# Kernel tuning notes

Measured on AMD Instinct MI355X. Metric: run time of the kernel, lower is better.

Reference implementation:

```python
import jax, jax.numpy as jnp
import numpy as np

N = 50000        # nodes
E = 1_600_000    # edges (avg degree 32)
IN_DIM = 128
NUM_CONFS = 16
CONF_EMB = 4
HIDDEN = 64
OUT = 32


def setup_inputs() -> dict:
    key = jax.random.key(0)
    ks = jax.random.split(key, 8)
    x = jax.random.normal(ks[0], (N, IN_DIM), jnp.float32)
    conf_ids = jax.random.randint(ks[1], (N,), 0, NUM_CONFS)
    edge_index = jax.random.randint(ks[2], (2, E), 0, N)
    edge_weight = jax.random.uniform(ks[3], (E,), jnp.float32)
    # learned params
    conf_table = jax.random.normal(ks[4], (NUM_CONFS, CONF_EMB), jnp.float32) * 0.1
    W1 = jax.random.normal(ks[5], (IN_DIM + CONF_EMB, HIDDEN), jnp.float32) / np.sqrt(IN_DIM + CONF_EMB)
    b1 = jnp.zeros((HIDDEN,), jnp.float32)
    W2 = jax.random.normal(ks[6], (HIDDEN, OUT), jnp.float32) / np.sqrt(HIDDEN)
    b2 = jnp.zeros((OUT,), jnp.float32)
    return dict(x=x, conf_ids=conf_ids, edge_index=edge_index, edge_weight=edge_weight,
                conf_table=conf_table, W1=W1, b1=b1, W2=W2, b2=b2)


def _gcn_conv(h, W, b, row, col, w, n):
    """PyG GCNConv: symmetric norm with self-loops (loops already appended to row/col/w)."""
    deg = jax.ops.segment_sum(w, col, num_segments=n)              # weighted in-degree [N]
    dinv = jnp.where(deg > 0, jax.lax.rsqrt(deg), 0.0)             # D^{-1/2}
    norm = dinv[row] * w * dinv[col]                               # per-edge coefficient [E+N]
    hW = h @ W                                                     # [N, out]
    out = jax.ops.segment_sum(hW[row] * norm[:, None], col, num_segments=n)
    return out + b


def reference(x, conf_ids, edge_index, edge_weight, conf_table, W1, b1, W2, b2):
    row, col = edge_index[0], edge_index[1]
    # add self-loops once (same math for both conv layers)
    loop = jnp.arange(N)
    row = jnp.concatenate([row, loop])
    col = jnp.concatenate([col, loop])
    w = jnp.concatenate([edge_weight, jnp.ones((N,), edge_weight.dtype)])

    h = jnp.concatenate([x, conf_table[conf_ids]], axis=-1)        # [N, in+conf_emb]
    h = jax.nn.relu(_gcn_conv(h, W1, b1, row, col, w, N))
    return _gcn_conv(h, W2, b2, row, col, w, N)
```

## Files before the change

### kernel.cpp

```cpp
#include <hip/hip_runtime.h>
#include <hip/hip_fp16.h>

#define WSCALE   65535.0f
#define BKT_SHIFT 8
#define BKT_SIZE  256
#define SEGCAP    10240
#define EPB       4096
#define EPT       16
#define NT        64

__global__ void k_binA(const int* __restrict__ row, const int* __restrict__ col,
                       const float* __restrict__ w, int* __restrict__ cursor,
                       uint2* __restrict__ seg, int e) {
    __shared__ int hist[256];
    __shared__ int base[256];
    __shared__ int rank[256];
    int t = threadIdx.x;
    hist[t] = 0; rank[t] = 0;
    __syncthreads();
    int b0 = blockIdx.x * EPB;
    unsigned pay[EPT]; unsigned cc[EPT];
#pragma unroll
    for (int k = 0; k < EPT; ++k) {
        int i = b0 + k * 256 + t;
        if (i < e) {
            unsigned r  = (unsigned)row[i];
            unsigned c  = (unsigned)col[i];
            unsigned wq = __float2uint_rn(w[i] * WSCALE);
            pay[k] = r | (wq << 16);
            cc[k] = c;
            atomicAdd(&hist[c >> BKT_SHIFT], 1);
        } else cc[k] = 0xFFFFFFFFu;
    }
    __syncthreads();
    if (hist[t] > 0) base[t] = atomicAdd(&cursor[t], hist[t]);
    __syncthreads();
#pragma unroll
    for (int k = 0; k < EPT; ++k) {
        if (cc[k] != 0xFFFFFFFFu) {
            int b = cc[k] >> BKT_SHIFT;
            int pos = base[b] + atomicAdd(&rank[b], 1);
            if (pos < SEGCAP)
                seg[(size_t)b * SEGCAP + pos] = make_uint2(pay[k], cc[k] & (BKT_SIZE - 1));
        }
    }
}

__global__ void k_binB(const int* __restrict__ cursor, const uint2* __restrict__ seg,
                       unsigned* __restrict__ csr, int* __restrict__ begs,
                       int* __restrict__ cnts, float* __restrict__ dinv, int n) {
    __shared__ int hist[BKT_SIZE];
    __shared__ unsigned wsum[BKT_SIZE];
    __shared__ int begL[BKT_SIZE];
    __shared__ int rank[BKT_SIZE];
    __shared__ unsigned pay[SEGCAP];
    int b = blockIdx.x;
    int t = threadIdx.x;
    int nodes = min(BKT_SIZE, n - b * BKT_SIZE);
    int count = min(cursor[b], SEGCAP);
    hist[t] = 0; wsum[t] = 0; rank[t] = 0;
    __syncthreads();
    const uint2* sp = seg + (size_t)b * SEGCAP;
    for (int i = t; i < count; i += 256) {
        uint2 r = sp[i];
        atomicAdd(&hist[r.y], 1);
        atomicAdd(&wsum[r.y], r.x >> 16);
    }
    __syncthreads();
    int v = hist[t];
    begL[t] = v;
    __syncthreads();
    for (int off = 1; off < 256; off <<= 1) {
        int tv = 0;
        if (t >= off) tv = begL[t - off];
        __syncthreads();
        begL[t] += tv;
        __syncthreads();
    }
    int beg_excl = begL[t] - v;
    __syncthreads();
    begL[t] = beg_excl;
    __syncthreads();
    if (t < nodes) {
        int node = b * BKT_SIZE + t;
        begs[node] = b * SEGCAP + beg_excl;
        cnts[node] = v;
        dinv[node] = rsqrtf(1.0f + (float)wsum[t] * (1.0f / WSCALE));
    }
    for (int i = t; i < count; i += 256) {
        uint2 r = sp[i];
        int pos = begL[r.y] + atomicAdd(&rank[r.y], 1);
        pay[pos] = r.x;
    }
    __syncthreads();
    unsigned* cp = csr + (size_t)b * SEGCAP;
    for (int i = t; i < count; i += 256) cp[i] = pay[i];
}

__global__ void k_hw1(const float* __restrict__ x, const int* __restrict__ conf_ids,
                      const float* __restrict__ conf_table, const float* __restrict__ W1,
                      const float* __restrict__ dinv, __half* __restrict__ hW1s, int n) {
    __shared__ float xs[NT][128];
    __shared__ float cemb[NT][4];
    int t = threadIdx.x;
    int base = blockIdx.x * NT;
    for (int q = t; q < NT * 32; q += 256) {
        int node = base + (q >> 5);
        int k4 = (q & 31) * 4;
        float4 v = make_float4(0.f, 0.f, 0.f, 0.f);
        if (node < n) v = *(const float4*)(x + (size_t)node * 128 + k4);
        *(float4*)&xs[q >> 5][k4] = v;
    }
    if (t < NT) {
        int node = base + t;
        int cid = (node < n) ? conf_ids[node] : 0;
        float4 ce = *(const float4*)(conf_table + cid * 4);
        if (node >= n) ce = make_float4(0.f, 0.f, 0.f, 0.f);
        *(float4*)&cemb[t][0] = ce;
    }
    __syncthreads();
    int w = t >> 6, f = t & 63;
    int nb = w * 16;
    float acc[16];
#pragma unroll
    for (int m = 0; m < 16; ++m) acc[m] = 0.f;
    for (int kq = 0; kq < 32; ++kq) {
        int k = kq * 4;
        float w1a = W1[(k + 0) * 64 + f];
        float w1b = W1[(k + 1) * 64 + f];
        float w1c = W1[(k + 2) * 64 + f];
        float w1d = W1[(k + 3) * 64 + f];
#pragma unroll
        for (int m = 0; m < 16; ++m) {
            float4 xv = *(const float4*)&xs[nb + m][k];
            acc[m] += xv.x * w1a + xv.y * w1b + xv.z * w1c + xv.w * w1d;
        }
    }
    float wca = W1[128 * 64 + f], wcb = W1[129 * 64 + f];
    float wcc = W1[130 * 64 + f], wcd = W1[131 * 64 + f];
#pragma unroll
    for (int m = 0; m < 16; ++m) {
        float4 ce = *(const float4*)&cemb[nb + m][0];
        acc[m] += ce.x * wca + ce.y * wcb + ce.z * wcc + ce.w * wcd;
    }
#pragma unroll
    for (int m = 0; m < 16; ++m) {
        int node = base + nb + m;
        if (node < n) hW1s[(size_t)node * 64 + f] = __float2half_rn(acc[m] * dinv[node]);
    }
}

__global__ void k_agg1(const __half* __restrict__ hW1s, const int* __restrict__ begs,
                       const int* __restrict__ cnts, const unsigned* __restrict__ csr,
                       const float* __restrict__ dinv, const float* __restrict__ b1,
                       const float* __restrict__ W2, __half* __restrict__ hW2s, int n) {
    __shared__ float h1s[8][64];
    int t = threadIdx.x;
    int q  = t >> 5;
    int hl = t & 31;
    int nid = blockIdx.x * 8 + q;
    const half2* __restrict__ hrow = (const half2*)hW1s;
    float a0 = 0.f, a1 = 0.f, dn = 0.f;
    float2 sf = make_float2(0.f, 0.f);
    int c = 0;
    const unsigned* sp = csr;
    if (nid < n) {
        dn = dinv[nid];
        c = cnts[nid];
        sp = csr + begs[nid];
        sf = __half22float2(hrow[(size_t)nid * 32 + hl]);
    }
    int cmax = max(c, __shfl_xor(c, 32));
    int j = 0;
    for (; j + 4 <= cmax; j += 4) {
        unsigned s0 = sp[j], s1 = sp[j + 1], s2 = sp[j + 2], s3 = sp[j + 3];
        float w0 = (j + 0 < c) ? (float)(s0 >> 16) : 0.f;
        float w1 = (j + 1 < c) ? (float)(s1 >> 16) : 0.f;
        float w2 = (j + 2 < c) ? (float)(s2 >> 16) : 0.f;
        float w3 = (j + 3 < c) ? (float)(s3 >> 16) : 0.f;
        float2 v0 = __half22float2(hrow[(size_t)(s0 & 0xffffu) * 32 + hl]);
        float2 v1 = __half22float2(hrow[(size_t)(s1 & 0xffffu) * 32 + hl]);
        float2 v2 = __half22float2(hrow[(size_t)(s2 & 0xffffu) * 32 + hl]);
        float2 v3 = __half22float2(hrow[(size_t)(s3 & 0xffffu) * 32 + hl]);
        a0 += v0.x * w0 + v1.x * w1 + v2.x * w2 + v3.x * w3;
        a1 += v0.y * w0 + v1.y * w1 + v2.y * w2 + v3.y * w3;
    }
    for (; j < cmax; ++j) {
        unsigned s = sp[j];
        float ww = (j < c) ? (float)(s >> 16) : 0.f;
        float2 v = __half22float2(hrow[(size_t)(s & 0xffffu) * 32 + hl]);
        a0 += v.x * ww;
        a1 += v.y * ww;
    }
    float2 bb = *(const float2*)(b1 + 2 * hl);
    float h0 = fmaxf((sf.x + a0 * (1.0f / WSCALE)) * dn + bb.x, 0.0f);
    float h1v = fmaxf((sf.y + a1 * (1.0f / WSCALE)) * dn + bb.y, 0.0f);
    if (nid >= n) { h0 = 0.f; h1v = 0.f; }
    *(float2*)&h1s[q][2 * hl] = make_float2(h0, h1v);
    __syncthreads();
    float s = 0.f;
#pragma unroll
    for (int k = 0; k < 64; k += 4) {
        float4 hv = *(const float4*)&h1s[q][k];
        s += hv.x * W2[(k + 0) * 32 + hl];
        s += hv.y * W2[(k + 1) * 32 + hl];
        s += hv.z * W2[(k + 2) * 32 + hl];
        s += hv.w * W2[(k + 3) * 32 + hl];
    }
    if (nid < n) hW2s[(size_t)nid * 32 + hl] = __float2half_rn(s * dn);
}

__global__ void k_agg2(const __half* __restrict__ hW2s, const int* __restrict__ begs,
                       const int* __restrict__ cnts, const unsigned* __restrict__ csr,
                       const float* __restrict__ dinv, const float* __restrict__ b2,
                       float* __restrict__ out, int n) {
    int t = threadIdx.x;
    int g  = t >> 4;
    int hl = t & 15;
    int nid = blockIdx.x * 16 + g;
    const half2* __restrict__ hrow = (const half2*)hW2s;
    float a0 = 0.f, a1 = 0.f, dn = 0.f;
    float2 sf = make_float2(0.f, 0.f);
    int c = 0;
    const unsigned* sp = csr;
    if (nid < n) {
        dn = dinv[nid];
        c = cnts[nid];
        sp = csr + begs[nid];
        sf = __half22float2(hrow[(size_t)nid * 16 + hl]);
    }
    int cmax = max(c, __shfl_xor(c, 16));
    cmax = max(cmax, __shfl_xor(cmax, 32));
    int j = 0;
    for (; j + 4 <= cmax; j += 4) {
        unsigned s0 = sp[j], s1 = sp[j + 1], s2 = sp[j + 2], s3 = sp[j + 3];
        float w0 = (j + 0 < c) ? (float)(s0 >> 16) : 0.f;
        float w1 = (j + 1 < c) ? (float)(s1 >> 16) : 0.f;
        float w2 = (j + 2 < c) ? (float)(s2 >> 16) : 0.f;
        float w3 = (j + 3 < c) ? (float)(s3 >> 16) : 0.f;
        float2 v0 = __half22float2(hrow[(size_t)(s0 & 0xffffu) * 16 + hl]);
        float2 v1 = __half22float2(hrow[(size_t)(s1 & 0xffffu) * 16 + hl]);
        float2 v2 = __half22float2(hrow[(size_t)(s2 & 0xffffu) * 16 + hl]);
        float2 v3 = __half22float2(hrow[(size_t)(s3 & 0xffffu) * 16 + hl]);
        a0 += v0.x * w0 + v1.x * w1 + v2.x * w2 + v3.x * w3;
        a1 += v0.y * w0 + v1.y * w1 + v2.y * w2 + v3.y * w3;
    }
    for (; j < cmax; ++j) {
        unsigned s = sp[j];
        float ww = (j < c) ? (float)(s >> 16) : 0.f;
        float2 v = __half22float2(hrow[(size_t)(s & 0xffffu) * 16 + hl]);
        a0 += v.x * ww;
        a1 += v.y * ww;
    }
    if (nid < n) {
        float2 bb = *(const float2*)(b2 + 2 * hl);
        float o0 = (sf.x + a0 * (1.0f / WSCALE)) * dn + bb.x;
        float o1 = (sf.y + a1 * (1.0f / WSCALE)) * dn + bb.y;
        *(float2*)&out[(size_t)nid * 32 + 2 * hl] = make_float2(o0, o1);
    }
}

extern "C" void kernel_launch(void* const* d_in, const int* in_sizes, int n_in,
                              void* d_out, int out_size, void* d_ws, size_t ws_size,
                              hipStream_t stream) {
    const float* x          = (const float*)d_in[0];
    const int*   conf_ids   = (const int*)  d_in[1];
    const int*   eidx       = (const int*)  d_in[2];
    const float* ew         = (const float*)d_in[3];
    const float* conf_table = (const float*)d_in[4];
    const float* W1         = (const float*)d_in[5];
    const float* b1         = (const float*)d_in[6];
    const float* W2         = (const float*)d_in[7];
    const float* b2         = (const float*)d_in[8];
    float* out = (float*)d_out;

    const int n = in_sizes[1];
    const int e = in_sizes[3];
    const int* row = eidx;
    const int* col = eidx + e;
    const int nbkt = (n + BKT_SIZE - 1) / BKT_SIZE;

    char* ws = (char*)d_ws;
    size_t off = 0;
    auto alloc = [&](size_t bytes) -> char* {
        char* p = ws + off;
        off = (off + bytes + 255) & ~(size_t)255;
        return p;
    };
    int*      cursor = (int*)     alloc(256 * 4);
    uint2*    seg    = (uint2*)   alloc((size_t)nbkt * SEGCAP * 8);
    unsigned* csr    = (unsigned*)alloc((size_t)nbkt * SEGCAP * 4);
    int*      begs   = (int*)     alloc((size_t)n * 4);
    int*      cnts   = (int*)     alloc((size_t)n * 4);
    float*    dinv   = (float*)   alloc((size_t)n * 4);
    __half*   hW2s   = (__half*)  alloc((size_t)n * 32 * 2);
    __half*   hW1s   = (__half*)seg;

    const int B = 256;
    int ga  = (e + EPB - 1) / EPB;
    int gt  = (n + NT - 1) / NT;
    int g8  = (n + 7) / 8;
    int g16 = (n + 15) / 16;

    hipMemsetAsync(cursor, 0, 256 * 4, stream);
    k_binA<<<ga,   B, 0, stream>>>(row, col, ew, cursor, seg, e);
    k_binB<<<nbkt, B, 0, stream>>>(cursor, seg, csr, begs, cnts, dinv, n);
    k_hw1 <<<gt,   B, 0, stream>>>(x, conf_ids, conf_table, W1, dinv, hW1s, n);
    k_agg1<<<g8,   B, 0, stream>>>(hW1s, begs, cnts, csr, dinv, b1, W2, hW2s, n);
    k_agg2<<<g16,  B, 0, stream>>>(hW2s, begs, cnts, csr, dinv, b2, out, n);
}
```

Baseline: 145.1 us.

## Pad CSR rows to multiples of 8 and aggregate with fp16 weights and packed FMA

Edge weights are now stored as fp16 bits instead of 16-bit fixed point, so the gather loops can do half2 FMAs without an int-to-float conversion. Each node's CSR row is zero-padded to a multiple of 8 entries, which allows 16-byte uint4 loads of the edge list with one-block prefetch and removes per-edge bounds masks and the cross-lane max of counts. The costs are less accumulation precision from fp16 partial sums over 8 edges, extra padded CSR storage and writes, and possible over-reads past the segment end during prefetch.

Result: faster. 135.7 us (-6.5%).

```diff
diff --git a/kernel.cpp b/kernel.cpp
--- a/kernel.cpp
+++ b/kernel.cpp
@@ -1,7 +1,6 @@
 #include <hip/hip_runtime.h>
 #include <hip/hip_fp16.h>
 
-#define WSCALE   65535.0f
 #define BKT_SHIFT 8
 #define BKT_SIZE  256
 #define SEGCAP    10240
@@ -26,7 +25,7 @@
         if (i < e) {
             unsigned r  = (unsigned)row[i];
             unsigned c  = (unsigned)col[i];
-            unsigned wq = __float2uint_rn(w[i] * WSCALE);
+            unsigned wq = (unsigned)__half_as_ushort(__float2half_rn(w[i]));
             pay[k] = r | (wq << 16);
             cc[k] = c;
             atomicAdd(&hist[c >> BKT_SHIFT], 1);
@@ -50,7 +49,7 @@
                        unsigned* __restrict__ csr, int* __restrict__ begs,
                        int* __restrict__ cnts, float* __restrict__ dinv, int n) {
     __shared__ int hist[BKT_SIZE];
-    __shared__ unsigned wsum[BKT_SIZE];
+    __shared__ float wsumf[BKT_SIZE];
     __shared__ int begL[BKT_SIZE];
     __shared__ int rank[BKT_SIZE];
     __shared__ unsigned pay[SEGCAP];
@@ -58,43 +57,46 @@
     int t = threadIdx.x;
     int nodes = min(BKT_SIZE, n - b * BKT_SIZE);
     int count = min(cursor[b], SEGCAP);
-    hist[t] = 0; wsum[t] = 0; rank[t] = 0;
+    hist[t] = 0; wsumf[t] = 0.f; rank[t] = 0;
     __syncthreads();
     const uint2* sp = seg + (size_t)b * SEGCAP;
     for (int i = t; i < count; i += 256) {
         uint2 r = sp[i];
         atomicAdd(&hist[r.y], 1);
-        atomicAdd(&wsum[r.y], r.x >> 16);
+        atomicAdd(&wsumf[r.y], __half2float(__ushort_as_half((unsigned short)(r.x >> 16))));
     }
     __syncthreads();
     int v = hist[t];
-    begL[t] = v;
+    int vpad = (v + 7) & ~7;
+    begL[t] = vpad;
     __syncthreads();
     for (int off = 1; off < 256; off <<= 1) {
-        int tv = 0;
-        if (t >= off) tv = begL[t - off];
+        int tv = (t >= off) ? begL[t - off] : 0;
         __syncthreads();
         begL[t] += tv;
         __syncthreads();
     }
-    int beg_excl = begL[t] - v;
+    int beg_excl = begL[t] - vpad;
+    int ptot = min(begL[255], SEGCAP);
     __syncthreads();
     begL[t] = beg_excl;
     __syncthreads();
     if (t < nodes) {
         int node = b * BKT_SIZE + t;
         begs[node] = b * SEGCAP + beg_excl;
-        cnts[node] = v;
-        dinv[node] = rsqrtf(1.0f + (float)wsum[t] * (1.0f / WSCALE));
-    }
+        cnts[node] = vpad;
+        dinv[node] = rsqrtf(1.0f + wsumf[t]);
+    }
+    for (int i = t; i < ptot; i += 256) pay[i] = 0u;
+    __syncthreads();
     for (int i = t; i < count; i += 256) {
         uint2 r = sp[i];
         int pos = begL[r.y] + atomicAdd(&rank[r.y], 1);
-        pay[pos] = r.x;
+        if (pos < SEGCAP) pay[pos] = r.x;
     }
     __syncthreads();
     unsigned* cp = csr + (size_t)b * SEGCAP;
-    for (int i = t; i < count; i += 256) cp[i] = pay[i];
+    for (int i = t; i < ptot; i += 256) cp[i] = pay[i];
 }
 
 __global__ void k_hw1(const float* __restrict__ x, const int* __restrict__ conf_ids,
@@ -160,7 +162,7 @@
     int hl = t & 31;
     int nid = blockIdx.x * 8 + q;
     const half2* __restrict__ hrow = (const half2*)hW1s;
-    float a0 = 0.f, a1 = 0.f, dn = 0.f;
+    float dn = 0.f;
     float2 sf = make_float2(0.f, 0.f);
     int c = 0;
     const unsigned* sp = csr;
@@ -170,31 +172,29 @@
         sp = csr + begs[nid];
         sf = __half22float2(hrow[(size_t)nid * 32 + hl]);
     }
-    int cmax = max(c, __shfl_xor(c, 32));
-    int j = 0;
-    for (; j + 4 <= cmax; j += 4) {
-        unsigned s0 = sp[j], s1 = sp[j + 1], s2 = sp[j + 2], s3 = sp[j + 3];
-        float w0 = (j + 0 < c) ? (float)(s0 >> 16) : 0.f;
-        float w1 = (j + 1 < c) ? (float)(s1 >> 16) : 0.f;
-        float w2 = (j + 2 < c) ? (float)(s2 >> 16) : 0.f;
-        float w3 = (j + 3 < c) ? (float)(s3 >> 16) : 0.f;
-        float2 v0 = __half22float2(hrow[(size_t)(s0 & 0xffffu) * 32 + hl]);
-        float2 v1 = __half22float2(hrow[(size_t)(s1 & 0xffffu) * 32 + hl]);
-        float2 v2 = __half22float2(hrow[(size_t)(s2 & 0xffffu) * 32 + hl]);
-        float2 v3 = __half22float2(hrow[(size_t)(s3 & 0xffffu) * 32 + hl]);
-        a0 += v0.x * w0 + v1.x * w1 + v2.x * w2 + v3.x * w3;
-        a1 += v0.y * w0 + v1.y * w1 + v2.y * w2 + v3.y * w3;
-    }
-    for (; j < cmax; ++j) {
-        unsigned s = sp[j];
-        float ww = (j < c) ? (float)(s >> 16) : 0.f;
-        float2 v = __half22float2(hrow[(size_t)(s & 0xffffu) * 32 + hl]);
-        a0 += v.x * ww;
-        a1 += v.y * ww;
+    float a0 = 0.f, a1 = 0.f;
+    const half2 hz = __float2half2_rn(0.f);
+    uint4 sa = *(const uint4*)(sp);
+    uint4 sb = *(const uint4*)(sp + 4);
+    for (int j = 0; j < c; j += 8) {
+        uint4 na = *(const uint4*)(sp + j + 8);
+        uint4 nb = *(const uint4*)(sp + j + 12);
+        half2 acc0 = hz, acc1 = hz;
+#define STEP1(s, A) { half2 vv = hrow[(size_t)((s) & 0xffffu) * 32 + hl]; \
+                      half2 ww = __half2half2(__ushort_as_half((unsigned short)((s) >> 16))); \
+                      A = __hfma2(vv, ww, A); }
+        STEP1(sa.x, acc0) STEP1(sa.y, acc1) STEP1(sa.z, acc0) STEP1(sa.w, acc1)
+        STEP1(sb.x, acc0) STEP1(sb.y, acc1) STEP1(sb.z, acc0) STEP1(sb.w, acc1)
+#undef STEP1
+        float2 f0 = __half22float2(acc0);
+        float2 f1 = __half22float2(acc1);
+        a0 += f0.x + f1.x;
+        a1 += f0.y + f1.y;
+        sa = na; sb = nb;
     }
     float2 bb = *(const float2*)(b1 + 2 * hl);
-    float h0 = fmaxf((sf.x + a0 * (1.0f / WSCALE)) * dn + bb.x, 0.0f);
-    float h1v = fmaxf((sf.y + a1 * (1.0f / WSCALE)) * dn + bb.y, 0.0f);
+    float h0  = fmaxf((sf.x + a0) * dn + bb.x, 0.0f);
+    float h1v = fmaxf((sf.y + a1) * dn + bb.y, 0.0f);
     if (nid >= n) { h0 = 0.f; h1v = 0.f; }
     *(float2*)&h1s[q][2 * hl] = make_float2(h0, h1v);
     __syncthreads();
@@ -219,7 +219,7 @@
     int hl = t & 15;
     int nid = blockIdx.x * 16 + g;
     const half2* __restrict__ hrow = (const half2*)hW2s;
-    float a0 = 0.f, a1 = 0.f, dn = 0.f;
+    float dn = 0.f;
     float2 sf = make_float2(0.f, 0.f);
     int c = 0;
     const unsigned* sp = csr;
@@ -229,33 +229,30 @@
         sp = csr + begs[nid];
         sf = __half22float2(hrow[(size_t)nid * 16 + hl]);
     }
-    int cmax = max(c, __shfl_xor(c, 16));
-    cmax = max(cmax, __shfl_xor(cmax, 32));
-    int j = 0;
-    for (; j + 4 <= cmax; j += 4) {
-        unsigned s0 = sp[j], s1 = sp[j + 1], s2 = sp[j + 2], s3 = sp[j + 3];
-        float w0 = (j + 0 < c) ? (float)(s0 >> 16) : 0.f;
-        float w1 = (j + 1 < c) ? (float)(s1 >> 16) : 0.f;
-        float w2 = (j + 2 < c) ? (float)(s2 >> 16) : 0.f;
-        float w3 = (j + 3 < c) ? (float)(s3 >> 16) : 0.f;
-        float2 v0 = __half22float2(hrow[(size_t)(s0 & 0xffffu) * 16 + hl]);
-        float2 v1 = __half22float2(hrow[(size_t)(s1 & 0xffffu) * 16 + hl]);
-        float2 v2 = __half22float2(hrow[(size_t)(s2 & 0xffffu) * 16 + hl]);
-        float2 v3 = __half22float2(hrow[(size_t)(s3 & 0xffffu) * 16 + hl]);
-        a0 += v0.x * w0 + v1.x * w1 + v2.x * w2 + v3.x * w3;
-        a1 += v0.y * w0 + v1.y * w1 + v2.y * w2 + v3.y * w3;
-    }
-    for (; j < cmax; ++j) {
-        unsigned s = sp[j];
-        float ww = (j < c) ? (float)(s >> 16) : 0.f;
-        float2 v = __half22float2(hrow[(size_t)(s & 0xffffu) * 16 + hl]);
-        a0 += v.x * ww;
-        a1 += v.y * ww;
+    float a0 = 0.f, a1 = 0.f;
+    const half2 hz = __float2half2_rn(0.f);
+    uint4 sa = *(const uint4*)(sp);
+    uint4 sb = *(const uint4*)(sp + 4);
+    for (int j = 0; j < c; j += 8) {
+        uint4 na = *(const uint4*)(sp + j + 8);
+        uint4 nb = *(const uint4*)(sp + j + 12);
+        half2 acc0 = hz, acc1 = hz;
+#define STEP2(s, A) { half2 vv = hrow[(size_t)((s) & 0xffffu) * 16 + hl]; \
+                      half2 ww = __half2half2(__ushort_as_half((unsigned short)((s) >> 16))); \
+                      A = __hfma2(vv, ww, A); }
+        STEP2(sa.x, acc0) STEP2(sa.y, acc1) STEP2(sa.z, acc0) STEP2(sa.w, acc1)
+        STEP2(sb.x, acc0) STEP2(sb.y, acc1) STEP2(sb.z, acc0) STEP2(sb.w, acc1)
+#undef STEP2
+        float2 f0 = __half22float2(acc0);
+        float2 f1 = __half22float2(acc1);
+        a0 += f0.x + f1.x;
+        a1 += f0.y + f1.y;
+        sa = na; sb = nb;
     }
     if (nid < n) {
         float2 bb = *(const float2*)(b2 + 2 * hl);
-        float o0 = (sf.x + a0 * (1.0f / WSCALE)) * dn + bb.x;
-        float o1 = (sf.y + a1 * (1.0f / WSCALE)) * dn + bb.y;
+        float o0 = (sf.x + a0) * dn + bb.x;
+        float o1 = (sf.y + a1) * dn + bb.y;
         *(float2*)&out[(size_t)nid * 32 + 2 * hl] = make_float2(o0, o1);
     }
 }
```
